# Kernel tuning notes

Measured on AMD Instinct MI355X. Metric: run time of the kernel, lower is better.

## Reference

```python
import jax, jax.numpy as jnp
import numpy as np
import math

TAU = 1.0  # init kwarg tau


def setup_inputs() -> dict:
    key = jax.random.key(0)
    n, m = 1024, 8192
    V = jax.random.normal(key, (n, m), dtype=jnp.float32)
    return {"V": V}


def reference(V) -> jnp.ndarray:
    n, m = V.shape
    num_rounds = math.ceil(m / n)
    # Repeat V row-blocks num_rounds times: M has shape [num_rounds*n, m]
    M = jnp.tile(V, (num_rounds, 1))

    def step(c, row):
        # Soft round-robin pick (training branch of SoftRR.__one_round)
        y = jax.nn.softmax((row - jnp.min(row) + 1.0) * c / TAU)
        c = (1.0 - y) * c
        return c, y

    c0 = jnp.ones((m,), dtype=V.dtype)
    _, R = jax.lax.scan(step, c0, M)  # R: [num_rounds*n, m]
    pi = R.reshape(num_rounds, n, m).sum(axis=0)  # [n, m]
    return pi
```

## Files before the change

kernel.cpp:

```cpp
#include <hip/hip_runtime.h>
#include <hip/hip_fp16.h>


#define N_ROWS 1024
#define M_COLS 8192
#define STEPS  8192
#define LOG2E  1.4426950408889634f

using half8  = __attribute__((ext_vector_type(8))) _Float16;
using half2v = __attribute__((ext_vector_type(2))) _Float16;

__device__ __forceinline__ float fast_exp2(float x) {
#if __has_builtin(__builtin_amdgcn_exp2f)
  return __builtin_amdgcn_exp2f(x);
#else
  return exp2f(x);
#endif
}
__device__ __forceinline__ float fast_rcp(float x) {
#if __has_builtin(__builtin_amdgcn_rcpf)
  return __builtin_amdgcn_rcpf(x);
#else
  return 1.0f / x;
#endif
}
__device__ __forceinline__ half2v pack_f16(float y0, float y1) {
  return __builtin_bit_cast(half2v, __builtin_amdgcn_cvt_pkrtz(y0, y1));
}

template <int CTRL>
__device__ __forceinline__ float dpp_add(float x) {
  int yi = __builtin_amdgcn_update_dpp(0, __builtin_bit_cast(int, x),
                                       CTRL, 0xf, 0xf, true);
  return x + __builtin_bit_cast(float, yi);
}

__device__ __forceinline__ float wave_sum_to_lane63(float x) {
  x = dpp_add<0x111>(x);
  x = dpp_add<0x112>(x);
  x = dpp_add<0x114>(x);
  x = dpp_add<0x118>(x);
  x = dpp_add<0x142>(x);
  x = dpp_add<0x143>(x);
  return x;
}

#define BAR_LDS_ONLY() asm volatile("s_waitcnt lgkmcnt(0)\n\ts_barrier" ::: "memory")

__global__ void softrr_rowmin(const float* __restrict__ V, float* __restrict__ rmin) {
  const int row = blockIdx.x;
  const float* p = V + (size_t)row * M_COLS;
  float m = 1e30f;
  for (int j = threadIdx.x; j < M_COLS; j += 256) m = fminf(m, p[j]);
#pragma unroll
  for (int off = 32; off; off >>= 1) m = fminf(m, __shfl_xor(m, off, 64));
  __shared__ float sm[4];
  if ((threadIdx.x & 63) == 0) sm[threadIdx.x >> 6] = m;
  __syncthreads();
  if (threadIdx.x == 0) {
    rmin[row] = fminf(fminf(sm[0], sm[1]), fminf(sm[2], sm[3]));
  }
}

__global__ void softrr_prep(const float* __restrict__ V, const float* __restrict__ rmin,
                            __half* __restrict__ A) {
  const int idx8 = blockIdx.x * 256 + threadIdx.x;
  const int row = idx8 >> 10;
  const float mn = rmin[row];
  const float4* v4 = (const float4*)V;
  float4 va = v4[2 * idx8];
  float4 vb = v4[2 * idx8 + 1];
  half8 o;
  o[0] = (_Float16)((va.x - mn + 1.0f) * LOG2E);
  o[1] = (_Float16)((va.y - mn + 1.0f) * LOG2E);
  o[2] = (_Float16)((va.z - mn + 1.0f) * LOG2E);
  o[3] = (_Float16)((va.w - mn + 1.0f) * LOG2E);
  o[4] = (_Float16)((vb.x - mn + 1.0f) * LOG2E);
  o[5] = (_Float16)((vb.y - mn + 1.0f) * LOG2E);
  o[6] = (_Float16)((vb.z - mn + 1.0f) * LOG2E);
  o[7] = (_Float16)((vb.w - mn + 1.0f) * LOG2E);
  ((half8*)A)[idx8] = o;
}

__device__ __forceinline__ void rr_step(
    int s,
    const half8& acur, half8& adst,
    float (&e)[8], float (&c)[8], half8& o,
    const half8* __restrict__ A8, half8* __restrict__ R8,
    float (*sP)[16], int t, int lane, int wave)
{
  const int par = s & 1;
  float x = (lane < 16) ? sP[par][lane] : 0.0f;

  R8[(size_t)((s - 1) & (STEPS - 1)) * 1024 + t] = o;

  adst = A8[((s + 3) & (N_ROWS - 1)) * 1024 + t];

  x = dpp_add<0x111>(x);
  x = dpp_add<0x112>(x);
  x = dpp_add<0x114>(x);
  x = dpp_add<0x118>(x);
  const float S = __builtin_bit_cast(
      float, __builtin_amdgcn_readlane(__builtin_bit_cast(int, x), 15));
  const float Sinv = fast_rcp(S);

  float y[8];
#pragma unroll
  for (int k = 0; k < 8; ++k) {
    y[k] = e[k] * Sinv;
    c[k] = __builtin_fmaf(-y[k], c[k], c[k]);
    e[k] = fast_exp2(__builtin_fmaf((float)acur[k], c[k], 0.0f));
  }
  float l = ((e[0] + e[1]) + (e[2] + e[3])) + ((e[4] + e[5]) + (e[6] + e[7]));
  l = wave_sum_to_lane63(l);
  if (lane == 63) sP[par ^ 1][wave] = l;

  {
    half2v h0 = pack_f16(y[0], y[1]);
    half2v h1 = pack_f16(y[2], y[3]);
    half2v h2 = pack_f16(y[4], y[5]);
    half2v h3 = pack_f16(y[6], y[7]);
    o[0] = h0[0]; o[1] = h0[1]; o[2] = h1[0]; o[3] = h1[1];
    o[4] = h2[0]; o[5] = h2[1]; o[6] = h3[0]; o[7] = h3[1];
  }
  BAR_LDS_ONLY();
}

__global__ void __launch_bounds__(1024) softrr_scan_nor(const __half* __restrict__ Ah,
                                                        __half* __restrict__ Rh) {
  const int t = threadIdx.x;
  const int wave = t >> 6;
  const int lane = t & 63;
  __shared__ float sP[2][16];

  const half8* __restrict__ A8 = (const half8*)Ah;
  half8* __restrict__ R8 = (half8*)Rh;

  float c[8], e[8];
#pragma unroll
  for (int k = 0; k < 8; ++k) c[k] = 1.0f;

  half8 r0 = A8[t];
  half8 pA = A8[1024 + t];
  half8 pB = A8[2048 + t];
  half8 pC, pD;

#pragma unroll
  for (int k = 0; k < 8; ++k) e[k] = fast_exp2((float)r0[k]);
  {
    float l = ((e[0] + e[1]) + (e[2] + e[3])) + ((e[4] + e[5]) + (e[6] + e[7]));
    l = wave_sum_to_lane63(l);
    if (lane == 63) sP[0][wave] = l;
  }
  half8 o;
  {
    half2v z = pack_f16(0.0f, 0.0f);
    o[0]=z[0]; o[1]=z[1]; o[2]=z[0]; o[3]=z[1];
    o[4]=z[0]; o[5]=z[1]; o[6]=z[0]; o[7]=z[1];
  }
  BAR_LDS_ONLY();

  for (int s = 0; s < STEPS; s += 4) {
    rr_step(s + 0, pA, pC, e, c, o, A8, R8, sP, t, lane, wave);
    rr_step(s + 1, pB, pD, e, c, o, A8, R8, sP, t, lane, wave);
    rr_step(s + 2, pC, pA, e, c, o, A8, R8, sP, t, lane, wave);
    rr_step(s + 3, pD, pB, e, c, o, A8, R8, sP, t, lane, wave);
  }

  R8[(size_t)(STEPS - 1) * 1024 + t] = o;
}

__global__ void softrr_sum8(const __half* __restrict__ Rh, float* __restrict__ out) {
  const int idx8 = blockIdx.x * 256 + threadIdx.x;
  const half8* R8 = (const half8*)Rh;
  float acc[8];
  {
    half8 v = R8[idx8];
#pragma unroll
    for (int k = 0; k < 8; ++k) acc[k] = (float)v[k];
  }
#pragma unroll
  for (int r = 1; r < 8; ++r) {
    half8 v = R8[(size_t)r * 1024 * 1024 + idx8];
#pragma unroll
    for (int k = 0; k < 8; ++k) acc[k] += (float)v[k];
  }
  ((float4*)out)[2 * idx8]     = make_float4(acc[0], acc[1], acc[2], acc[3]);
  ((float4*)out)[2 * idx8 + 1] = make_float4(acc[4], acc[5], acc[6], acc[7]);
}

__global__ void __launch_bounds__(512) softrr_scan_a(const __half* __restrict__ Ah,
                                                     __half* __restrict__ PIh) {
  const int t = threadIdx.x;
  const int wave = t >> 6;
  const int lane = t & 63;
  __shared__ float sP[2][8];
  const half8* __restrict__ A8 = (const half8*)Ah;
  half8* __restrict__ P8 = (half8*)PIh;
  float c[16];
#pragma unroll
  for (int k = 0; k < 16; ++k) c[k] = 1.0f;
  half8 a0 = A8[2 * t];
  half8 a1 = A8[2 * t + 1];
  half8 p0, p1;
  for (int s = 0; s < STEPS; ++s) {
    const int i = s & (N_ROWS - 1);
    const int r = s >> 10;
    const int in_ = (s + 1) & (N_ROWS - 1);
    const int par = s & 1;
    half8 an0 = A8[in_ * 1024 + 2 * t];
    half8 an1 = A8[in_ * 1024 + 2 * t + 1];
    float e[16];
#pragma unroll
    for (int k = 0; k < 8; ++k) {
      e[k]     = fast_exp2((float)a0[k] * c[k]);
      e[8 + k] = fast_exp2((float)a1[k] * c[8 + k]);
    }
    float l = (((e[0] + e[1]) + (e[2] + e[3])) + ((e[4] + e[5]) + (e[6] + e[7])))
            + (((e[8] + e[9]) + (e[10] + e[11])) + ((e[12] + e[13]) + (e[14] + e[15])));
    l = wave_sum_to_lane63(l);
    if (lane == 63) sP[par][wave] = l;
    BAR_LDS_ONLY();
    float x = (lane < 8) ? sP[par][lane] : 0.0f;
    x = dpp_add<0x111>(x);
    x = dpp_add<0x112>(x);
    x = dpp_add<0x114>(x);
    const float S = __builtin_bit_cast(
        float, __builtin_amdgcn_readlane(__builtin_bit_cast(int, x), 7));
    const float Sinv = fast_rcp(S);
    half8 o0, o1;
#pragma unroll
    for (int k = 0; k < 8; k += 2) {
      float y0 = e[k] * Sinv, y1 = e[k + 1] * Sinv;
      c[k] = __builtin_fmaf(-y0, c[k], c[k]);
      c[k + 1] = __builtin_fmaf(-y1, c[k + 1], c[k + 1]);
      half2v h = pack_f16(y0, y1);
      o0[k] = h[0]; o0[k + 1] = h[1];
    }
#pragma unroll
    for (int k = 0; k < 8; k += 2) {
      float y0 = e[8 + k] * Sinv, y1 = e[8 + k + 1] * Sinv;
      c[8 + k] = __builtin_fmaf(-y0, c[8 + k], c[8 + k]);
      c[8 + k + 1] = __builtin_fmaf(-y1, c[8 + k + 1], c[8 + k + 1]);
      half2v h = pack_f16(y0, y1);
      o1[k] = h[0]; o1[k + 1] = h[1];
    }
    if (r > 0) { o0 = o0 + p0; o1 = o1 + p1; }
    P8[i * 1024 + 2 * t]     = o0;
    P8[i * 1024 + 2 * t + 1] = o1;
    a0 = an0; a1 = an1;
    p0 = P8[in_ * 1024 + 2 * t];
    p1 = P8[in_ * 1024 + 2 * t + 1];
  }
}

__global__ void softrr_cvt(const __half* __restrict__ PIh, float* __restrict__ out) {
  const int idx8 = blockIdx.x * 256 + threadIdx.x;
  half8 p = ((const half8*)PIh)[idx8];
  ((float4*)out)[2 * idx8]     = make_float4((float)p[0], (float)p[1], (float)p[2], (float)p[3]);
  ((float4*)out)[2 * idx8 + 1] = make_float4((float)p[4], (float)p[5], (float)p[6], (float)p[7]);
}

__global__ void __launch_bounds__(1024) softrr_scan_b(const float* __restrict__ V,
                                                      const float* __restrict__ rmin,
                                                      float* __restrict__ out) {
  const int t = threadIdx.x;
  const int wave = t >> 6;
  const int lane = t & 63;
  __shared__ float partials[2][16];
  __shared__ float smin[N_ROWS];
  smin[t] = rmin[t];
  __syncthreads();
  const float4* __restrict__ V4 = (const float4*)V;
  float4* O4 = (float4*)out;
  float c[8];
#pragma unroll
  for (int k = 0; k < 8; ++k) c[k] = 1.0f;
  float4 va = V4[2 * t], vb = V4[2 * t + 1];
  float4 pa, pb;
  for (int s = 0; s < STEPS; ++s) {
    const int i = s & (N_ROWS - 1);
    const int r = s >> 10;
    const int in_ = (s + 1) & (N_ROWS - 1);
    float4 van = V4[in_ * 2048 + 2 * t];
    float4 vbn = V4[in_ * 2048 + 2 * t + 1];
    const float mn = smin[i];
    const float base = (1.0f - mn) * LOG2E;
    float vv[8] = {va.x, va.y, va.z, va.w, vb.x, vb.y, vb.z, vb.w};
    float e[8];
    float l = 0.0f;
#pragma unroll
    for (int k = 0; k < 8; ++k) {
      float zb = __builtin_fmaf(vv[k], LOG2E, base);
      e[k] = fast_exp2(zb * c[k]);
      l += e[k];
    }
#pragma unroll
    for (int off = 32; off; off >>= 1) l += __shfl_xor(l, off, 64);
    if (lane == 0) partials[s & 1][wave] = l;
    __syncthreads();
    float S = 0.0f;
#pragma unroll
    for (int w = 0; w < 16; ++w) S += partials[s & 1][w];
    const float Sinv = fast_rcp(S);
    float po[8] = {pa.x, pa.y, pa.z, pa.w, pb.x, pb.y, pb.z, pb.w};
    float o[8];
#pragma unroll
    for (int k = 0; k < 8; ++k) {
      float y = e[k] * Sinv;
      c[k] = __builtin_fmaf(-y, c[k], c[k]);
      o[k] = (r > 0) ? (po[k] + y) : y;
    }
    O4[i * 2048 + 2 * t]     = make_float4(o[0], o[1], o[2], o[3]);
    O4[i * 2048 + 2 * t + 1] = make_float4(o[4], o[5], o[6], o[7]);
    va = van; vb = vbn;
    pa = O4[in_ * 2048 + 2 * t];
    pb = O4[in_ * 2048 + 2 * t + 1];
  }
}

extern "C" void kernel_launch(void* const* d_in, const int* in_sizes, int n_in,
                              void* d_out, int out_size, void* d_ws, size_t ws_size,
                              hipStream_t stream) {
  const float* V = (const float*)d_in[0];
  float* out = (float*)d_out;
  float* rmin = (float*)d_ws;

  const size_t A_BYTES = (size_t)N_ROWS * M_COLS * 2;
  const size_t R_BYTES = (size_t)STEPS * M_COLS * 2;
  const size_t need_nor = 4096 + A_BYTES + R_BYTES;
  const size_t need_rmw = 4096 + A_BYTES + A_BYTES;

  if (ws_size >= need_nor) {
    __half* A = (__half*)((char*)d_ws + 4096);
    __half* R = (__half*)((char*)d_ws + 4096 + A_BYTES);
    softrr_rowmin<<<N_ROWS, 256, 0, stream>>>(V, rmin);
    softrr_prep<<<4096, 256, 0, stream>>>(V, rmin, A);
    softrr_scan_nor<<<1, 1024, 0, stream>>>(A, R);
    softrr_sum8<<<4096, 256, 0, stream>>>(R, out);
  } else if (ws_size >= need_rmw) {
    __half* A  = (__half*)((char*)d_ws + 4096);
    __half* PI = (__half*)((char*)d_ws + 4096 + A_BYTES);
    softrr_rowmin<<<N_ROWS, 256, 0, stream>>>(V, rmin);
    softrr_prep<<<4096, 256, 0, stream>>>(V, rmin, A);
    softrr_scan_a<<<1, 512, 0, stream>>>(A, PI);
    softrr_cvt<<<4096, 256, 0, stream>>>(PI, out);
  } else {
    softrr_rowmin<<<N_ROWS, 256, 0, stream>>>(V, rmin);
    softrr_scan_b<<<1, 1024, 0, stream>>>(V, rmin, out);
  }
}
```

Before: 4.288 ms.

## Use LDS atomic rotating sum slots and fp32 prescaled input in scan

Adds a new scan path that reads the prescaled input as fp32 instead of fp16, which drops the per-element half-to-float conversion. The per-step cross-wave sum now goes through LDS atomicAdd into a four-slot rotating buffer. Every thread then reads the total with one LDS load, replacing the 16-lane DPP reduction and readlane. The fp32 input doubles the workspace and the streamed read traffic for A. The RMW fallback path is removed, and the new path only runs when the workspace is large enough.

```diff
diff --git a/kernel.cpp b/kernel.cpp
--- a/kernel.cpp
+++ b/kernel.cpp
@@ -9,6 +9,7 @@
 
 using half8  = __attribute__((ext_vector_type(8))) _Float16;
 using half2v = __attribute__((ext_vector_type(2))) _Float16;
+using float8 = __attribute__((ext_vector_type(8))) float;
 
 __device__ __forceinline__ float fast_exp2(float x) {
 #if __has_builtin(__builtin_amdgcn_exp2f)
@@ -62,8 +63,28 @@
   }
 }
 
-__global__ void softrr_prep(const float* __restrict__ V, const float* __restrict__ rmin,
-                            __half* __restrict__ A) {
+__global__ void softrr_prep_f32(const float* __restrict__ V, const float* __restrict__ rmin,
+                                float* __restrict__ A) {
+  const int idx8 = blockIdx.x * 256 + threadIdx.x;
+  const int row = idx8 >> 10;
+  const float mn = rmin[row];
+  const float4* v4 = (const float4*)V;
+  float4 va = v4[2 * idx8];
+  float4 vb = v4[2 * idx8 + 1];
+  float8 o;
+  o[0] = (va.x - mn + 1.0f) * LOG2E;
+  o[1] = (va.y - mn + 1.0f) * LOG2E;
+  o[2] = (va.z - mn + 1.0f) * LOG2E;
+  o[3] = (va.w - mn + 1.0f) * LOG2E;
+  o[4] = (vb.x - mn + 1.0f) * LOG2E;
+  o[5] = (vb.y - mn + 1.0f) * LOG2E;
+  o[6] = (vb.z - mn + 1.0f) * LOG2E;
+  o[7] = (vb.w - mn + 1.0f) * LOG2E;
+  ((float8*)A)[idx8] = o;
+}
+
+__global__ void softrr_prep16(const float* __restrict__ V, const float* __restrict__ rmin,
+                              __half* __restrict__ A) {
   const int idx8 = blockIdx.x * 256 + threadIdx.x;
   const int row = idx8 >> 10;
   const float mn = rmin[row];
@@ -82,7 +103,92 @@
   ((half8*)A)[idx8] = o;
 }
 
+template <int POS>
 __device__ __forceinline__ void rr_step(
+    int s,
+    const float8& acur, float8& adst,
+    float (&e)[8], float (&c)[8], half8& o,
+    const float8* __restrict__ A8, half8* __restrict__ R8,
+    float* sS, int t, int lane, int wave)
+{
+  if (wave == 0) sS[(POS + 2) & 3] = 0.0f;
+  const float S = sS[(POS + 3) & 3];
+
+  R8[(size_t)((s - 1) & (STEPS - 1)) * 1024 + t] = o;
+  adst = A8[((s + 3) & (N_ROWS - 1)) * 1024 + t];
+
+  const float Sinv = fast_rcp(S);
+
+  float y[8];
+#pragma unroll
+  for (int k = 0; k < 8; ++k) {
+    y[k] = e[k] * Sinv;
+    c[k] = __builtin_fmaf(-y[k], c[k], c[k]);
+    e[k] = fast_exp2(acur[k] * c[k]);
+  }
+  float l = ((e[0] + e[1]) + (e[2] + e[3])) + ((e[4] + e[5]) + (e[6] + e[7]));
+  l = wave_sum_to_lane63(l);
+  if (lane == 63) atomicAdd(&sS[POS & 3], l);
+
+  {
+    half2v h0 = pack_f16(y[0], y[1]);
+    half2v h1 = pack_f16(y[2], y[3]);
+    half2v h2 = pack_f16(y[4], y[5]);
+    half2v h3 = pack_f16(y[6], y[7]);
+    o[0] = h0[0]; o[1] = h0[1]; o[2] = h1[0]; o[3] = h1[1];
+    o[4] = h2[0]; o[5] = h2[1]; o[6] = h3[0]; o[7] = h3[1];
+  }
+  BAR_LDS_ONLY();
+}
+
+__global__ void __launch_bounds__(1024) softrr_scan_f32(const float* __restrict__ Af,
+                                                        __half* __restrict__ Rh) {
+  const int t = threadIdx.x;
+  const int wave = t >> 6;
+  const int lane = t & 63;
+  __shared__ float sS[4];
+
+  const float8* __restrict__ A8 = (const float8*)Af;
+  half8* __restrict__ R8 = (half8*)Rh;
+
+  float c[8], e[8];
+#pragma unroll
+  for (int k = 0; k < 8; ++k) c[k] = 1.0f;
+
+  if (t < 4) sS[t] = 0.0f;
+  __syncthreads();
+
+  float8 r0 = A8[t];
+  float8 pA = A8[1024 + t];
+  float8 pB = A8[2048 + t];
+  float8 pC, pD;
+
+#pragma unroll
+  for (int k = 0; k < 8; ++k) e[k] = fast_exp2(r0[k]);
+  {
+    float l = ((e[0] + e[1]) + (e[2] + e[3])) + ((e[4] + e[5]) + (e[6] + e[7]));
+    l = wave_sum_to_lane63(l);
+    if (lane == 63) atomicAdd(&sS[3], l);
+  }
+  half8 o;
+  {
+    half2v z = pack_f16(0.0f, 0.0f);
+    o[0]=z[0]; o[1]=z[1]; o[2]=z[0]; o[3]=z[1];
+    o[4]=z[0]; o[5]=z[1]; o[6]=z[0]; o[7]=z[1];
+  }
+  BAR_LDS_ONLY();
+
+  for (int s = 0; s < STEPS; s += 4) {
+    rr_step<0>(s + 0, pA, pC, e, c, o, A8, R8, sS, t, lane, wave);
+    rr_step<1>(s + 1, pB, pD, e, c, o, A8, R8, sS, t, lane, wave);
+    rr_step<2>(s + 2, pC, pA, e, c, o, A8, R8, sS, t, lane, wave);
+    rr_step<3>(s + 3, pD, pB, e, c, o, A8, R8, sS, t, lane, wave);
+  }
+
+  R8[(size_t)(STEPS - 1) * 1024 + t] = o;
+}
+
+__device__ __forceinline__ void rr_step16(
     int s,
     const half8& acur, half8& adst,
     float (&e)[8], float (&c)[8], half8& o,
@@ -91,11 +197,8 @@
 {
   const int par = s & 1;
   float x = (lane < 16) ? sP[par][lane] : 0.0f;
-
   R8[(size_t)((s - 1) & (STEPS - 1)) * 1024 + t] = o;
-
   adst = A8[((s + 3) & (N_ROWS - 1)) * 1024 + t];
-
   x = dpp_add<0x111>(x);
   x = dpp_add<0x112>(x);
   x = dpp_add<0x114>(x);
@@ -103,7 +206,6 @@
   const float S = __builtin_bit_cast(
       float, __builtin_amdgcn_readlane(__builtin_bit_cast(int, x), 15));
   const float Sinv = fast_rcp(S);
-
   float y[8];
 #pragma unroll
   for (int k = 0; k < 8; ++k) {
@@ -114,7 +216,6 @@
   float l = ((e[0] + e[1]) + (e[2] + e[3])) + ((e[4] + e[5]) + (e[6] + e[7]));
   l = wave_sum_to_lane63(l);
   if (lane == 63) sP[par ^ 1][wave] = l;
-
   {
     half2v h0 = pack_f16(y[0], y[1]);
     half2v h1 = pack_f16(y[2], y[3]);
@@ -132,19 +233,15 @@
   const int wave = t >> 6;
   const int lane = t & 63;
   __shared__ float sP[2][16];
-
   const half8* __restrict__ A8 = (const half8*)Ah;
   half8* __restrict__ R8 = (half8*)Rh;
-
   float c[8], e[8];
 #pragma unroll
   for (int k = 0; k < 8; ++k) c[k] = 1.0f;
-
   half8 r0 = A8[t];
   half8 pA = A8[1024 + t];
   half8 pB = A8[2048 + t];
   half8 pC, pD;
-
 #pragma unroll
   for (int k = 0; k < 8; ++k) e[k] = fast_exp2((float)r0[k]);
   {
@@ -159,14 +256,12 @@
     o[4]=z[0]; o[5]=z[1]; o[6]=z[0]; o[7]=z[1];
   }
   BAR_LDS_ONLY();
-
   for (int s = 0; s < STEPS; s += 4) {
-    rr_step(s + 0, pA, pC, e, c, o, A8, R8, sP, t, lane, wave);
-    rr_step(s + 1, pB, pD, e, c, o, A8, R8, sP, t, lane, wave);
-    rr_step(s + 2, pC, pA, e, c, o, A8, R8, sP, t, lane, wave);
-    rr_step(s + 3, pD, pB, e, c, o, A8, R8, sP, t, lane, wave);
-  }
-
+    rr_step16(s + 0, pA, pC, e, c, o, A8, R8, sP, t, lane, wave);
+    rr_step16(s + 1, pB, pD, e, c, o, A8, R8, sP, t, lane, wave);
+    rr_step16(s + 2, pC, pA, e, c, o, A8, R8, sP, t, lane, wave);
+    rr_step16(s + 3, pD, pB, e, c, o, A8, R8, sP, t, lane, wave);
+  }
   R8[(size_t)(STEPS - 1) * 1024 + t] = o;
 }
 
@@ -187,78 +282,6 @@
   }
   ((float4*)out)[2 * idx8]     = make_float4(acc[0], acc[1], acc[2], acc[3]);
   ((float4*)out)[2 * idx8 + 1] = make_float4(acc[4], acc[5], acc[6], acc[7]);
-}
-
-__global__ void __launch_bounds__(512) softrr_scan_a(const __half* __restrict__ Ah,
-                                                     __half* __restrict__ PIh) {
-  const int t = threadIdx.x;
-  const int wave = t >> 6;
-  const int lane = t & 63;
-  __shared__ float sP[2][8];
-  const half8* __restrict__ A8 = (const half8*)Ah;
-  half8* __restrict__ P8 = (half8*)PIh;
-  float c[16];
-#pragma unroll
-  for (int k = 0; k < 16; ++k) c[k] = 1.0f;
-  half8 a0 = A8[2 * t];
-  half8 a1 = A8[2 * t + 1];
-  half8 p0, p1;
-  for (int s = 0; s < STEPS; ++s) {
-    const int i = s & (N_ROWS - 1);
-    const int r = s >> 10;
-    const int in_ = (s + 1) & (N_ROWS - 1);
-    const int par = s & 1;
-    half8 an0 = A8[in_ * 1024 + 2 * t];
-    half8 an1 = A8[in_ * 1024 + 2 * t + 1];
-    float e[16];
-#pragma unroll
-    for (int k = 0; k < 8; ++k) {
-      e[k]     = fast_exp2((float)a0[k] * c[k]);
-      e[8 + k] = fast_exp2((float)a1[k] * c[8 + k]);
-    }
-    float l = (((e[0] + e[1]) + (e[2] + e[3])) + ((e[4] + e[5]) + (e[6] + e[7])))
-            + (((e[8] + e[9]) + (e[10] + e[11])) + ((e[12] + e[13]) + (e[14] + e[15])));
-    l = wave_sum_to_lane63(l);
-    if (lane == 63) sP[par][wave] = l;
-    BAR_LDS_ONLY();
-    float x = (lane < 8) ? sP[par][lane] : 0.0f;
-    x = dpp_add<0x111>(x);
-    x = dpp_add<0x112>(x);
-    x = dpp_add<0x114>(x);
-    const float S = __builtin_bit_cast(
-        float, __builtin_amdgcn_readlane(__builtin_bit_cast(int, x), 7));
-    const float Sinv = fast_rcp(S);
-    half8 o0, o1;
-#pragma unroll
-    for (int k = 0; k < 8; k += 2) {
-      float y0 = e[k] * Sinv, y1 = e[k + 1] * Sinv;
-      c[k] = __builtin_fmaf(-y0, c[k], c[k]);
-      c[k + 1] = __builtin_fmaf(-y1, c[k + 1], c[k + 1]);
-      half2v h = pack_f16(y0, y1);
-      o0[k] = h[0]; o0[k + 1] = h[1];
-    }
-#pragma unroll
-    for (int k = 0; k < 8; k += 2) {
-      float y0 = e[8 + k] * Sinv, y1 = e[8 + k + 1] * Sinv;
-      c[8 + k] = __builtin_fmaf(-y0, c[8 + k], c[8 + k]);
-      c[8 + k + 1] = __builtin_fmaf(-y1, c[8 + k + 1], c[8 + k + 1]);
-      half2v h = pack_f16(y0, y1);
-      o1[k] = h[0]; o1[k + 1] = h[1];
-    }
-    if (r > 0) { o0 = o0 + p0; o1 = o1 + p1; }
-    P8[i * 1024 + 2 * t]     = o0;
-    P8[i * 1024 + 2 * t + 1] = o1;
-    a0 = an0; a1 = an1;
-    p0 = P8[in_ * 1024 + 2 * t];
-    p1 = P8[in_ * 1024 + 2 * t + 1];
-  }
-}
-
-__global__ void softrr_cvt(const __half* __restrict__ PIh, float* __restrict__ out) {
-  const int idx8 = blockIdx.x * 256 + threadIdx.x;
-  half8 p = ((const half8*)PIh)[idx8];
-  ((float4*)out)[2 * idx8]     = make_float4((float)p[0], (float)p[1], (float)p[2], (float)p[3]);
-  ((float4*)out)[2 * idx8 + 1] = make_float4((float)p[4], (float)p[5], (float)p[6], (float)p[7]);
 }
 
 __global__ void __launch_bounds__(1024) softrr_scan_b(const float* __restrict__ V,
@@ -326,25 +349,26 @@
   float* out = (float*)d_out;
   float* rmin = (float*)d_ws;
 
-  const size_t A_BYTES = (size_t)N_ROWS * M_COLS * 2;
-  const size_t R_BYTES = (size_t)STEPS * M_COLS * 2;
-  const size_t need_nor = 4096 + A_BYTES + R_BYTES;
-  const size_t need_rmw = 4096 + A_BYTES + A_BYTES;
-
-  if (ws_size >= need_nor) {
+  const size_t A16_BYTES = (size_t)N_ROWS * M_COLS * 2;
+  const size_t A32_BYTES = (size_t)N_ROWS * M_COLS * 4;
+  const size_t R_BYTES   = (size_t)STEPS * M_COLS * 2;
+  const size_t need_f32  = 4096 + A32_BYTES + R_BYTES;
+  const size_t need_nor  = 4096 + A16_BYTES + R_BYTES;
+
+  if (ws_size >= need_f32) {
+    float*  A = (float*)((char*)d_ws + 4096);
+    __half* R = (__half*)((char*)d_ws + 4096 + A32_BYTES);
+    softrr_rowmin<<<N_ROWS, 256, 0, stream>>>(V, rmin);
+    softrr_prep_f32<<<4096, 256, 0, stream>>>(V, rmin, A);
+    softrr_scan_f32<<<1, 1024, 0, stream>>>(A, R);
+    softrr_sum8<<<4096, 256, 0, stream>>>(R, out);
+  } else if (ws_size >= need_nor) {
     __half* A = (__half*)((char*)d_ws + 4096);
-    __half* R = (__half*)((char*)d_ws + 4096 + A_BYTES);
+    __half* R = (__half*)((char*)d_ws + 4096 + A16_BYTES);
     softrr_rowmin<<<N_ROWS, 256, 0, stream>>>(V, rmin);
-    softrr_prep<<<4096, 256, 0, stream>>>(V, rmin, A);
+    softrr_prep16<<<4096, 256, 0, stream>>>(V, rmin, A);
     softrr_scan_nor<<<1, 1024, 0, stream>>>(A, R);
     softrr_sum8<<<4096, 256, 0, stream>>>(R, out);
-  } else if (ws_size >= need_rmw) {
-    __half* A  = (__half*)((char*)d_ws + 4096);
-    __half* PI = (__half*)((char*)d_ws + 4096 + A_BYTES);
-    softrr_rowmin<<<N_ROWS, 256, 0, stream>>>(V, rmin);
-    softrr_prep<<<4096, 256, 0, stream>>>(V, rmin, A);
-    softrr_scan_a<<<1, 512, 0, stream>>>(A, PI);
-    softrr_cvt<<<4096, 256, 0, stream>>>(PI, out);
   } else {
     softrr_rowmin<<<N_ROWS, 256, 0, stream>>>(V, rmin);
     softrr_scan_b<<<1, 1024, 0, stream>>>(V, rmin, out);
```

New measurement: 4.865 ms. 1.13x slower.

## Replace per-step workgroup barrier with sequence-tagged LDS ring flags

Applied to the files above, without the earlier changes.

Removes the s_barrier from every scan step. Each wave now publishes its partial softmax sum to a 4-slot LDS ring as a 64-bit word that packs the step number with the value, and the reader lanes spin on atomic loads until all 16 waves' tags for the current step have arrived. This lets waves run somewhat decoupled instead of lockstepping, at the cost of polling traffic on LDS and a risk of slot reuse if a wave gets more than a few steps ahead. The unused read-modify-write fallback path is also removed.

```diff
diff --git a/kernel.cpp b/kernel.cpp
--- a/kernel.cpp
+++ b/kernel.cpp
@@ -24,8 +24,8 @@
   return 1.0f / x;
 #endif
 }
-__device__ __forceinline__ half2v pack_f16(float y0, float y1) {
-  return __builtin_bit_cast(half2v, __builtin_amdgcn_cvt_pkrtz(y0, y1));
+__device__ __forceinline__ unsigned pack_f16_u32(float y0, float y1) {
+  return __builtin_bit_cast(unsigned, __builtin_amdgcn_cvt_pkrtz(y0, y1));
 }
 
 template <int CTRL>
@@ -45,8 +45,6 @@
   return x;
 }
 
-#define BAR_LDS_ONLY() asm volatile("s_waitcnt lgkmcnt(0)\n\ts_barrier" ::: "memory")
-
 __global__ void softrr_rowmin(const float* __restrict__ V, float* __restrict__ rmin) {
   const int row = blockIdx.x;
   const float* p = V + (size_t)row * M_COLS;
@@ -62,8 +60,8 @@
   }
 }
 
-__global__ void softrr_prep(const float* __restrict__ V, const float* __restrict__ rmin,
-                            __half* __restrict__ A) {
+__global__ void softrr_prep16(const float* __restrict__ V, const float* __restrict__ rmin,
+                              __half* __restrict__ A) {
   const int idx8 = blockIdx.x * 256 + threadIdx.x;
   const int row = idx8 >> 10;
   const float mn = rmin[row];
@@ -82,19 +80,24 @@
   ((half8*)A)[idx8] = o;
 }
 
-__device__ __forceinline__ void rr_step(
+template <int POS>
+__device__ __forceinline__ void rr_step_df(
     int s,
     const half8& acur, half8& adst,
-    float (&e)[8], float (&c)[8], half8& o,
-    const half8* __restrict__ A8, half8* __restrict__ R8,
-    float (*sP)[16], int t, int lane, int wave)
+    float (&e)[8], float (&c)[8], uint4& o,
+    const half8* __restrict__ A8, uint4* __restrict__ R4,
+    unsigned long long (*ring)[16], int t, int lane, int wavei)
 {
-  const int par = s & 1;
-  float x = (lane < 16) ? sP[par][lane] : 0.0f;
-
-  R8[(size_t)((s - 1) & (STEPS - 1)) * 1024 + t] = o;
-
+  R4[(size_t)((s - 1) & (STEPS - 1)) * 1024 + t] = o;
   adst = A8[((s + 3) & (N_ROWS - 1)) * 1024 + t];
+
+  const unsigned want = (unsigned)(s + 1);
+  unsigned long long v;
+  do {
+    v = __hip_atomic_load(&ring[POS][lane & 15], __ATOMIC_RELAXED,
+                          __HIP_MEMORY_SCOPE_WORKGROUP);
+  } while ((unsigned)(v >> 32) != want);
+  float x = __uint_as_float((unsigned)v);
 
   x = dpp_add<0x111>(x);
   x = dpp_add<0x112>(x);
@@ -113,28 +116,32 @@
   }
   float l = ((e[0] + e[1]) + (e[2] + e[3])) + ((e[4] + e[5]) + (e[6] + e[7]));
   l = wave_sum_to_lane63(l);
-  if (lane == 63) sP[par ^ 1][wave] = l;
-
-  {
-    half2v h0 = pack_f16(y[0], y[1]);
-    half2v h1 = pack_f16(y[2], y[3]);
-    half2v h2 = pack_f16(y[4], y[5]);
-    half2v h3 = pack_f16(y[6], y[7]);
-    o[0] = h0[0]; o[1] = h0[1]; o[2] = h1[0]; o[3] = h1[1];
-    o[4] = h2[0]; o[5] = h2[1]; o[6] = h3[0]; o[7] = h3[1];
-  }
-  BAR_LDS_ONLY();
-}
-
-__global__ void __launch_bounds__(1024) softrr_scan_nor(const __half* __restrict__ Ah,
-                                                        __half* __restrict__ Rh) {
+  if (lane == 63) {
+    const unsigned long long pv =
+        ((unsigned long long)(unsigned)(s + 2) << 32) |
+        (unsigned long long)__builtin_bit_cast(unsigned, l);
+    __hip_atomic_store(&ring[(POS + 1) & 3][wavei], pv, __ATOMIC_RELAXED,
+                       __HIP_MEMORY_SCOPE_WORKGROUP);
+  }
+
+  o.x = pack_f16_u32(y[0], y[1]);
+  o.y = pack_f16_u32(y[2], y[3]);
+  o.z = pack_f16_u32(y[4], y[5]);
+  o.w = pack_f16_u32(y[6], y[7]);
+}
+
+__global__ void __launch_bounds__(1024) softrr_scan_df(const __half* __restrict__ Ah,
+                                                       __half* __restrict__ Rh) {
   const int t = threadIdx.x;
-  const int wave = t >> 6;
+  const int wavei = t >> 6;
   const int lane = t & 63;
-  __shared__ float sP[2][16];
+  __shared__ unsigned long long ring[4][16];
 
   const half8* __restrict__ A8 = (const half8*)Ah;
-  half8* __restrict__ R8 = (half8*)Rh;
+  uint4* __restrict__ R4 = (uint4*)Rh;
+
+  if (t < 64) ring[t >> 4][t & 15] = 0ULL;
+  __syncthreads();
 
   float c[8], e[8];
 #pragma unroll
@@ -150,24 +157,23 @@
   {
     float l = ((e[0] + e[1]) + (e[2] + e[3])) + ((e[4] + e[5]) + (e[6] + e[7]));
     l = wave_sum_to_lane63(l);
-    if (lane == 63) sP[0][wave] = l;
-  }
-  half8 o;
-  {
-    half2v z = pack_f16(0.0f, 0.0f);
-    o[0]=z[0]; o[1]=z[1]; o[2]=z[0]; o[3]=z[1];
-    o[4]=z[0]; o[5]=z[1]; o[6]=z[0]; o[7]=z[1];
-  }
-  BAR_LDS_ONLY();
+    if (lane == 63) {
+      const unsigned long long pv =
+          (1ULL << 32) | (unsigned long long)__builtin_bit_cast(unsigned, l);
+      __hip_atomic_store(&ring[0][wavei], pv, __ATOMIC_RELAXED,
+                         __HIP_MEMORY_SCOPE_WORKGROUP);
+    }
+  }
+  uint4 o = make_uint4(0u, 0u, 0u, 0u);
 
   for (int s = 0; s < STEPS; s += 4) {
-    rr_step(s + 0, pA, pC, e, c, o, A8, R8, sP, t, lane, wave);
-    rr_step(s + 1, pB, pD, e, c, o, A8, R8, sP, t, lane, wave);
-    rr_step(s + 2, pC, pA, e, c, o, A8, R8, sP, t, lane, wave);
-    rr_step(s + 3, pD, pB, e, c, o, A8, R8, sP, t, lane, wave);
-  }
-
-  R8[(size_t)(STEPS - 1) * 1024 + t] = o;
+    rr_step_df<0>(s + 0, pA, pC, e, c, o, A8, R4, ring, t, lane, wavei);
+    rr_step_df<1>(s + 1, pB, pD, e, c, o, A8, R4, ring, t, lane, wavei);
+    rr_step_df<2>(s + 2, pC, pA, e, c, o, A8, R4, ring, t, lane, wavei);
+    rr_step_df<3>(s + 3, pD, pB, e, c, o, A8, R4, ring, t, lane, wavei);
+  }
+
+  R4[(size_t)(STEPS - 1) * 1024 + t] = o;
 }
 
 __global__ void softrr_sum8(const __half* __restrict__ Rh, float* __restrict__ out) {
@@ -187,78 +193,6 @@
   }
   ((float4*)out)[2 * idx8]     = make_float4(acc[0], acc[1], acc[2], acc[3]);
   ((float4*)out)[2 * idx8 + 1] = make_float4(acc[4], acc[5], acc[6], acc[7]);
-}
-
-__global__ void __launch_bounds__(512) softrr_scan_a(const __half* __restrict__ Ah,
-                                                     __half* __restrict__ PIh) {
-  const int t = threadIdx.x;
-  const int wave = t >> 6;
-  const int lane = t & 63;
-  __shared__ float sP[2][8];
-  const half8* __restrict__ A8 = (const half8*)Ah;
-  half8* __restrict__ P8 = (half8*)PIh;
-  float c[16];
-#pragma unroll
-  for (int k = 0; k < 16; ++k) c[k] = 1.0f;
-  half8 a0 = A8[2 * t];
-  half8 a1 = A8[2 * t + 1];
-  half8 p0, p1;
-  for (int s = 0; s < STEPS; ++s) {
-    const int i = s & (N_ROWS - 1);
-    const int r = s >> 10;
-    const int in_ = (s + 1) & (N_ROWS - 1);
-    const int par = s & 1;
-    half8 an0 = A8[in_ * 1024 + 2 * t];
-    half8 an1 = A8[in_ * 1024 + 2 * t + 1];
-    float e[16];
-#pragma unroll
-    for (int k = 0; k < 8; ++k) {
-      e[k]     = fast_exp2((float)a0[k] * c[k]);
-      e[8 + k] = fast_exp2((float)a1[k] * c[8 + k]);
-    }
-    float l = (((e[0] + e[1]) + (e[2] + e[3])) + ((e[4] + e[5]) + (e[6] + e[7])))
-            + (((e[8] + e[9]) + (e[10] + e[11])) + ((e[12] + e[13]) + (e[14] + e[15])));
-    l = wave_sum_to_lane63(l);
-    if (lane == 63) sP[par][wave] = l;
-    BAR_LDS_ONLY();
-    float x = (lane < 8) ? sP[par][lane] : 0.0f;
-    x = dpp_add<0x111>(x);
-    x = dpp_add<0x112>(x);
-    x = dpp_add<0x114>(x);
-    const float S = __builtin_bit_cast(
-        float, __builtin_amdgcn_readlane(__builtin_bit_cast(int, x), 7));
-    const float Sinv = fast_rcp(S);
-    half8 o0, o1;
-#pragma unroll
-    for (int k = 0; k < 8; k += 2) {
-      float y0 = e[k] * Sinv, y1 = e[k + 1] * Sinv;
-      c[k] = __builtin_fmaf(-y0, c[k], c[k]);
-      c[k + 1] = __builtin_fmaf(-y1, c[k + 1], c[k + 1]);
-      half2v h = pack_f16(y0, y1);
-      o0[k] = h[0]; o0[k + 1] = h[1];
-    }
-#pragma unroll
-    for (int k = 0; k < 8; k += 2) {
-      float y0 = e[8 + k] * Sinv, y1 = e[8 + k + 1] * Sinv;
-      c[8 + k] = __builtin_fmaf(-y0, c[8 + k], c[8 + k]);
-      c[8 + k + 1] = __builtin_fmaf(-y1, c[8 + k + 1], c[8 + k + 1]);
-      half2v h = pack_f16(y0, y1);
-      o1[k] = h[0]; o1[k + 1] = h[1];
-    }
-    if (r > 0) { o0 = o0 + p0; o1 = o1 + p1; }
-    P8[i * 1024 + 2 * t]     = o0;
-    P8[i * 1024 + 2 * t + 1] = o1;
-    a0 = an0; a1 = an1;
-    p0 = P8[in_ * 1024 + 2 * t];
-    p1 = P8[in_ * 1024 + 2 * t + 1];
-  }
-}
-
-__global__ void softrr_cvt(const __half* __restrict__ PIh, float* __restrict__ out) {
-  const int idx8 = blockIdx.x * 256 + threadIdx.x;
-  half8 p = ((const half8*)PIh)[idx8];
-  ((float4*)out)[2 * idx8]     = make_float4((float)p[0], (float)p[1], (float)p[2], (float)p[3]);
-  ((float4*)out)[2 * idx8 + 1] = make_float4((float)p[4], (float)p[5], (float)p[6], (float)p[7]);
 }
 
 __global__ void __launch_bounds__(1024) softrr_scan_b(const float* __restrict__ V,
@@ -326,25 +260,17 @@
   float* out = (float*)d_out;
   float* rmin = (float*)d_ws;
 
-  const size_t A_BYTES = (size_t)N_ROWS * M_COLS * 2;
-  const size_t R_BYTES = (size_t)STEPS * M_COLS * 2;
-  const size_t need_nor = 4096 + A_BYTES + R_BYTES;
-  const size_t need_rmw = 4096 + A_BYTES + A_BYTES;
-
-  if (ws_size >= need_nor) {
+  const size_t A16_BYTES = (size_t)N_ROWS * M_COLS * 2;
+  const size_t R_BYTES   = (size_t)STEPS * M_COLS * 2;
+  const size_t need_df   = 4096 + A16_BYTES + R_BYTES;
+
+  if (ws_size >= need_df) {
     __half* A = (__half*)((char*)d_ws + 4096);
-    __half* R = (__half*)((char*)d_ws + 4096 + A_BYTES);
+    __half* R = (__half*)((char*)d_ws + 4096 + A16_BYTES);
     softrr_rowmin<<<N_ROWS, 256, 0, stream>>>(V, rmin);
-    softrr_prep<<<4096, 256, 0, stream>>>(V, rmin, A);
-    softrr_scan_nor<<<1, 1024, 0, stream>>>(A, R);
+    softrr_prep16<<<4096, 256, 0, stream>>>(V, rmin, A);
+    softrr_scan_df<<<1, 1024, 0, stream>>>(A, R);
     softrr_sum8<<<4096, 256, 0, stream>>>(R, out);
-  } else if (ws_size >= need_rmw) {
-    __half* A  = (__half*)((char*)d_ws + 4096);
-    __half* PI = (__half*)((char*)d_ws + 4096 + A_BYTES);
-    softrr_rowmin<<<N_ROWS, 256, 0, stream>>>(V, rmin);
-    softrr_prep<<<4096, 256, 0, stream>>>(V, rmin, A);
-    softrr_scan_a<<<1, 512, 0, stream>>>(A, PI);
-    softrr_cvt<<<4096, 256, 0, stream>>>(PI, out);
   } else {
     softrr_rowmin<<<N_ROWS, 256, 0, stream>>>(V, rmin);
     softrr_scan_b<<<1, 1024, 0, stream>>>(V, rmin, out);
```

Result: slower. 4.436 ms (+3.5%).
